# Optimization experiments

Measured on AMD Instinct MI355X. Metric: run time of the kernel, lower is better.

## Reference

```python
import jax, jax.numpy as jnp
import numpy as np

N, T, CIN = 40000, 32, 8
VW = 64          # back_voxelwise_channels
P = 16           # v2b_maxvoxels (voxels stacked per BEV cell)
BEV_H, BEV_W = 496, 432
EPS = 1e-5


def _bn(key, shape):
    # returns stacked (gamma, beta, running_mean, running_var) along axis -2
    k1, k2, k3 = jax.random.split(key, 3)
    g = 1.0 + 0.1 * jax.random.normal(k1, shape, jnp.float32)
    b = 0.1 * jax.random.normal(k2, shape, jnp.float32)
    m = 0.1 * jax.random.normal(k3, shape, jnp.float32)
    v = jnp.ones(shape, jnp.float32)
    return jnp.stack([g, b, m, v], axis=-2)


def setup_inputs() -> dict:
    key = jax.random.key(0)
    ks = jax.random.split(key, 20)
    features = jax.random.normal(ks[0], (N, T, CIN), jnp.float32)
    cy = jax.random.randint(ks[1], (N, 1), 0, BEV_H)
    cx = jax.random.randint(ks[2], (N, 1), 0, BEV_W)
    coors = jnp.concatenate([cy, cx], axis=1).astype(jnp.int32)
    num_voxels = jax.random.randint(ks[3], (N,), 1, T + 1).astype(jnp.int32)

    def w(k, o, i):
        return jax.random.normal(k, (o, i), jnp.float32) / float(np.sqrt(i))

    return dict(
        features=features, coors=coors, num_voxels=num_voxels,
        vfe1_W=w(ks[4], 8, CIN), vfe1_bn=_bn(ks[5], (8,)),
        vfe2_W=w(ks[6], 32, 16), vfe2_bn=_bn(ks[7], (32,)),
        vfe3_W=w(ks[8], 64, 64), vfe3_bn=_bn(ks[9], (64,)),
        vfe4_W=w(ks[10], 64, 64), vfe4_bn=_bn(ks[11], (64,)),
        bfe1_W=jax.random.normal(ks[12], (16, P, P), jnp.float32) / float(np.sqrt(P)),
        bfe1_bn=_bn(ks[13], (16, P)),
        bfe2_W=jax.random.normal(ks[14], (16, 2, P), jnp.float32) / float(np.sqrt(P)),
        bfe2_bn=_bn(ks[15], (16, 2)),
        bfe3_W=w(ks[16], 128, 128), bfe3_bn=_bn(ks[17], (128,)),
    )


def _forward(features, vfe1_W, vfe1_bn, vfe2_W, vfe2_bn, vfe3_W, vfe3_bn,
             vfe4_W, vfe4_bn, bfe1_W, bfe1_bn, bfe2_W, bfe2_bn, bfe3_W, bfe3_bn,
             coors, num_voxels):
    n, t = features.shape[0], features.shape[1]
    f32 = features.dtype
    mask = (jnp.arange(t)[None, :] < num_voxels[:, None]).astype(f32)[..., None]  # [N,T,1]

    def fe(x, W, bn):  # Linear (no bias) + BatchNorm1d (eval) + Mish
        g, b, m, v = bn
        y = x @ W.T
        y = (y - m) * jax.lax.rsqrt(v + EPS) * g + b
        return y * jnp.tanh(jax.nn.softplus(y))

    def vfe(x, W, bn):  # pointwise FE, max-pool over points, concat
        p = fe(x, W, bn)
        agg = jnp.max(p, axis=1, keepdims=True)
        return jnp.concatenate([p, jnp.broadcast_to(agg, p.shape)], axis=2)

    x1 = vfe(features, vfe1_W, vfe1_bn)           # [N,T,16]
    x2 = vfe(x1, vfe2_W, vfe2_bn) * mask          # [N,T,64]
    x3 = fe(x2, vfe3_W, vfe3_bn)
    x4 = fe(x3, vfe4_W, vfe4_bn) * mask + x2
    voxelwise = jnp.max(x4, axis=1)               # [N,64]

    # ---- voxel2bev: group voxels by BEV cell, stack up to P per cell ----
    cell = coors[:, 0] * BEV_W + coors[:, 1]                         # [N]
    ucell, inv = jnp.unique(cell, return_inverse=True, size=n, fill_value=BEV_H * BEV_W)
    order = jnp.argsort(inv)                                          # stable
    inv_sorted = inv[order]
    pos_sorted = jnp.arange(n) - jnp.searchsorted(inv_sorted, inv_sorted, side='left')
    slot = jnp.zeros(n, jnp.int32).at[order].set(pos_sorted.astype(jnp.int32))
    row = jnp.where(slot < P, inv, n)                                 # overflow -> dropped
    bevs = jnp.zeros((n, P, VW), f32).at[row, jnp.minimum(slot, P - 1)].set(
        voxelwise, mode='drop')                                       # [N,P,64]
    counts = jax.ops.segment_sum(jnp.ones(n, jnp.int32), inv, num_segments=n)
    numv = jnp.minimum(counts, P)
    bevcoors = jnp.stack([ucell // BEV_W, ucell % BEV_W], axis=1)     # [N,2]

    # ---- 16 grouped FE stacks over the slot dimension ----
    x0 = bevs.transpose(0, 2, 1).reshape(n, 16, 4, P)                 # [N,16,4,P]
    m2 = (jnp.arange(P)[None, :] < numv[:, None]).astype(f32)[:, None, None, :]
    y = jnp.einsum('ngip,gqp->ngiq', x0, bfe1_W)                      # [N,16,4,P]
    g1, b1, m1, v1 = (bfe1_bn[None, :, i, None, :] for i in range(4))
    y = (y - m1) * jax.lax.rsqrt(v1 + EPS) * g1 + b1
    y = y * jnp.tanh(jax.nn.softplus(y)) * m2
    z = jnp.einsum('ngip,gcp->ngic', y, bfe2_W)                       # [N,16,4,2]
    g2, b2, m2b, v2 = (bfe2_bn[None, :, i, None, :] for i in range(4))
    z = (z - m2b) * jax.lax.rsqrt(v2 + EPS) * g2 + b2
    z = z * jnp.tanh(jax.nn.softplus(z))
    # torch cat along dim=-1 then view -> layout [N, 4, 16, 2] flattened
    x17 = z.transpose(0, 2, 1, 3).reshape(n, 128)
    x18 = fe(x17, bfe3_W, bfe3_bn)
    x19 = fe(x18, bfe3_W, bfe3_bn)   # original applies bfe3 twice (bfe4 unused)

    bevmap = jnp.zeros((BEV_H, BEV_W, 128), f32).at[
        bevcoors[:, 0], bevcoors[:, 1]].set(x19, mode='drop')
    return bevmap.transpose(2, 1, 0)                                  # [128, W, H]


def reference(features, coors, num_voxels, vfe1_W, vfe1_bn, vfe2_W, vfe2_bn,
              vfe3_W, vfe3_bn, vfe4_W, vfe4_bn, bfe1_W, bfe1_bn, bfe2_W, bfe2_bn,
              bfe3_W, bfe3_bn):
    return _forward(features, vfe1_W, vfe1_bn, vfe2_W, vfe2_bn, vfe3_W, vfe3_bn,
                    vfe4_W, vfe4_bn, bfe1_W, bfe1_bn, bfe2_W, bfe2_bn,
                    bfe3_W, bfe3_bn, coors, num_voxels)
```

## Files before the change

### kernel.cpp

```cpp
#include <hip/hip_runtime.h>

#define BEVW 432
#define BEVH 496
#define NCELL (BEVW*BEVH)
#define NVOX  40000
#define EPSB  1e-5f

typedef float f32x2 __attribute__((ext_vector_type(2)));
typedef float f32x4 __attribute__((ext_vector_type(4)));
typedef unsigned int u32x4 __attribute__((ext_vector_type(4)));
typedef short bf16x8 __attribute__((ext_vector_type(8)));

#define REP8_0(M)  M(0) M(1) M(2) M(3) M(4) M(5) M(6) M(7)
#define REP8_8(M)  M(8) M(9) M(10) M(11) M(12) M(13) M(14) M(15)
#define REP16_0(M)  REP8_0(M)  REP8_8(M)


__device__ __forceinline__ float mishf(float y) {
    float e = __expf(fminf(y, 40.f));
    float n = e * (e + 2.f);
    return y * n * __builtin_amdgcn_rcpf(n + 2.f);
}

template <int CTRL>
__device__ __forceinline__ float dppmaxf(float a) {
    int p = __builtin_amdgcn_update_dpp(0, __float_as_int(a), CTRL, 0xF, 0xF, true);
    return fmaxf(a, __int_as_float(p));
}
#define WMAX32(a) { \
    a = dppmaxf<0xB1>(a); \
    a = dppmaxf<0x4E>(a); \
    a = dppmaxf<0x141>(a); \
    a = dppmaxf<0x140>(a); \
    a = fmaxf(a, __int_as_float(__builtin_amdgcn_ds_swizzle(__float_as_int(a), 0x401F))); }

__device__ __forceinline__ bf16x8 mkbf8(uint a, uint b, uint c, uint d) {
    u32x4 t = {a, b, c, d};
    return __builtin_bit_cast(bf16x8, t);
}

__device__ __forceinline__ uint splitbf(float x) {
    uint rh = __float_as_uint(x) & 0xFFFF0000u;
    float lof = x - __uint_as_float(rh);
    uint ul = __float_as_uint(lof);
    uint rl = (ul + 0x7FFFu + ((ul >> 16) & 1u)) >> 16;
    return (rh >> 16) | (rl << 16);
}

__global__ __launch_bounds__(256) void setup_kernel(
    const float* __restrict__ vbn1, const float* __restrict__ vbn2,
    const float* __restrict__ vbn3, const float* __restrict__ vbn4,
    const float* __restrict__ bbn1, const float* __restrict__ bbn2,
    const float* __restrict__ bbn3, const float* __restrict__ W4,
    const float* __restrict__ W3g, const float* __restrict__ W2g,
    float* __restrict__ fold, ushort* __restrict__ w4fh, ushort* __restrict__ w4fl,
    ushort* __restrict__ w3fh, ushort* __restrict__ w3fl,
    ushort* __restrict__ w2fh, ushort* __restrict__ w2fl)
{
    int tid = threadIdx.x;
    if (tid < 8)  { float s = vbn1[tid]/sqrtf(vbn1[24+tid]+EPSB);  fold[tid]      = s; fold[8+tid]   = vbn1[8+tid]  - vbn1[16+tid]*s; }
    if (tid < 32) { float s = vbn2[tid]/sqrtf(vbn2[96+tid]+EPSB);  fold[16+tid]   = s; fold[48+tid]  = vbn2[32+tid] - vbn2[64+tid]*s; }
    if (tid < 64) { float s = vbn3[tid]/sqrtf(vbn3[192+tid]+EPSB); fold[80+tid]   = s; fold[144+tid] = vbn3[64+tid] - vbn3[128+tid]*s; }
    if (tid < 64) { float s = vbn4[tid]/sqrtf(vbn4[192+tid]+EPSB); fold[208+tid]  = s; fold[272+tid] = vbn4[64+tid] - vbn4[128+tid]*s; }
    if (tid < 128){ float s = bbn3[tid]/sqrtf(bbn3[384+tid]+EPSB); fold[336+tid]  = s; fold[464+tid] = bbn3[128+tid]- bbn3[256+tid]*s; }
    { int g = tid >> 4, q = tid & 15;
      const float* b = bbn1 + g*64;
      float s = b[q]/sqrtf(b[48+q]+EPSB);
      fold[592+tid] = s; fold[848+tid] = b[16+q] - b[32+q]*s; }
    if (tid < 32) { int g = tid >> 1, c = tid & 1;
      const float* b = bbn2 + g*8;
      float s = b[c]/sqrtf(b[6+c]+EPSB);
      fold[1104+tid] = s; fold[1136+tid] = b[2+c] - b[4+c]*s; }

    for (int i = tid; i < 4096; i += 256) {
        int j = i & 7, ln = (i >> 3) & 63, nt = (i >> 9) & 3, kc = i >> 11;
        int n = (ln & 15) + nt*16;
        int k = kc*32 + (ln >> 4)*8 + j;
        {
            float val = W4[n*64 + k];
            uint u = splitbf(val);
            w4fh[i] = (ushort)(u & 0xFFFFu);
            w4fl[i] = (ushort)(u >> 16);
        }
        {
            float val = W3g[n*64 + k];
            uint u = splitbf(val);
            w3fh[i] = (ushort)(u & 0xFFFFu);
            w3fl[i] = (ushort)(u >> 16);
        }
    }

    for (int i = tid; i < 1024; i += 256) {
        int j = i & 7, ln = (i >> 3) & 63, nt = (i >> 9) & 1;
        int n = (ln & 15) + nt*16;
        int k = (ln >> 4)*8 + j;
        float val = (k < 16) ? W2g[n*16 + k] : 0.f;
        uint u = splitbf(val);
        w2fh[i] = (ushort)(u & 0xFFFFu);
        w2fl[i] = (ushort)(u >> 16);
    }
}

#define MF3(D, AH, AL, BH, BL) \
    D = __builtin_amdgcn_mfma_f32_16x16x32_bf16(AL, BH, D, 0, 0, 0); \
    D = __builtin_amdgcn_mfma_f32_16x16x32_bf16(AH, BL, D, 0, 0, 0); \
    D = __builtin_amdgcn_mfma_f32_16x16x32_bf16(AH, BH, D, 0, 0, 0);

#define LDA(SRCP, mt, AH, AL) { \
    const uint* ap_ = (SRCP) + ((lane & 15) + 16*(mt))*33 + quad*8; \
    uint u0 = ap_[0], u1 = ap_[1], u2 = ap_[2], u3 = ap_[3]; \
    uint u4 = ap_[4], u5 = ap_[5], u6 = ap_[6], u7 = ap_[7]; \
    AH = mkbf8(__builtin_amdgcn_perm(u1,u0,0x05040100), __builtin_amdgcn_perm(u3,u2,0x05040100), \
               __builtin_amdgcn_perm(u5,u4,0x05040100), __builtin_amdgcn_perm(u7,u6,0x05040100)); \
    AL = mkbf8(__builtin_amdgcn_perm(u1,u0,0x07060302), __builtin_amdgcn_perm(u3,u2,0x07060302), \
               __builtin_amdgcn_perm(u5,u4,0x07060302), __builtin_amdgcn_perm(u7,u6,0x07060302)); }

#define LDA2(SRCP, mt, AH, AL) { \
    const uint* ap_ = (SRCP) + ((lane & 15) + 16*(mt))*33 + (quad & 1)*8; \
    uint u0 = ap_[0], u1 = ap_[1], u2 = ap_[2], u3 = ap_[3]; \
    uint u4 = ap_[4], u5 = ap_[5], u6 = ap_[6], u7 = ap_[7]; \
    AH = mkbf8(__builtin_amdgcn_perm(u1,u0,0x05040100), __builtin_amdgcn_perm(u3,u2,0x05040100), \
               __builtin_amdgcn_perm(u5,u4,0x05040100), __builtin_amdgcn_perm(u7,u6,0x05040100)); \
    AL = mkbf8(__builtin_amdgcn_perm(u1,u0,0x07060302), __builtin_amdgcn_perm(u3,u2,0x07060302), \
               __builtin_amdgcn_perm(u5,u4,0x07060302), __builtin_amdgcn_perm(u7,u6,0x07060302)); }

#define LDB8(ARR, BHP, BLP) { \
    uint4 h0_=(BHP)[0], l0_=(BLP)[0], h1_=(BHP)[64], l1_=(BLP)[64]; \
    uint4 h2_=(BHP)[128], l2_=(BLP)[128], h3_=(BHP)[192], l3_=(BLP)[192]; \
    ARR[0]=mkbf8(h0_.x,h0_.y,h0_.z,h0_.w); ARR[1]=mkbf8(l0_.x,l0_.y,l0_.z,l0_.w); \
    ARR[2]=mkbf8(h1_.x,h1_.y,h1_.z,h1_.w); ARR[3]=mkbf8(l1_.x,l1_.y,l1_.z,l1_.w); \
    ARR[4]=mkbf8(h2_.x,h2_.y,h2_.z,h2_.w); ARR[5]=mkbf8(l2_.x,l2_.y,l2_.z,l2_.w); \
    ARR[6]=mkbf8(h3_.x,h3_.y,h3_.z,h3_.w); ARR[7]=mkbf8(l3_.x,l3_.y,l3_.z,l3_.w); }

#define TILE4A(SRCP, mt, BA, D0, D1, D2, D3) { \
    bf16x8 Ah_, Al_; LDA(SRCP, mt, Ah_, Al_) \
    MF3(D0, Ah_, Al_, BA[0], BA[1]) MF3(D1, Ah_, Al_, BA[2], BA[3]) \
    MF3(D2, Ah_, Al_, BA[4], BA[5]) MF3(D3, Ah_, Al_, BA[6], BA[7]) }

#define DOSETA(SRCP, BA, ACC, SKA, SKB) { \
    TILE4A(SRCP, 0, BA, ACC[0], ACC[1], ACC[2], ACC[3]) \
    TILE4A(SRCP, 2, BA, ACC[8], ACC[9], ACC[10], ACC[11]) \
    if (!(SKA)) { TILE4A(SRCP, 1, BA, ACC[4], ACC[5], ACC[6], ACC[7]) } \
    if (!(SKB)) { TILE4A(SRCP, 3, BA, ACC[12], ACC[13], ACC[14], ACC[15]) } }

__global__ __launch_bounds__(64, 3) void vfe_kernel(
    const float* __restrict__ feat, const int* __restrict__ coors,
    const int* __restrict__ nvx,
    const float* __restrict__ W1,
    const ushort* __restrict__ w2fh, const ushort* __restrict__ w2fl,
    const ushort* __restrict__ w3fh, const ushort* __restrict__ w3fl,
    const ushort* __restrict__ w4fh, const ushort* __restrict__ w4fl,
    const float* __restrict__ fold,
    float* __restrict__ voxelwise, int* __restrict__ cnt,
    int* __restrict__ list, int* __restrict__ nact, int* __restrict__ act)
{
    __shared__ char ldsbuf[16896];
    int tid = threadIdx.x;
    int lane = tid;
    int quad = lane >> 4;
    int c0 = lane & 15;
    int v = blockIdx.x * 2 + (tid >> 5);
    int vA = blockIdx.x * 2;
    int t = tid & 31;
    uint*  x2s  = (uint*)ldsbuf;
    uint*  x2s1 = x2s + 2112;

    const float* fp = feat + (v*32 + t)*8;
    float4 fa = *(const float4*)(fp);
    float4 fb = *(const float4*)(fp+4);
    int numv = nvx[v];
    bf16x8 Bw2[4];
    {
        const uint4* bh2 = (const uint4*)w2fh + lane;
        const uint4* bl2 = (const uint4*)w2fl + lane;
        uint4 h0_=bh2[0], l0_=bl2[0], h1_=bh2[64], l1_=bl2[64];
        Bw2[0]=mkbf8(h0_.x,h0_.y,h0_.z,h0_.w); Bw2[1]=mkbf8(l0_.x,l0_.y,l0_.z,l0_.w);
        Bw2[2]=mkbf8(h1_.x,h1_.y,h1_.z,h1_.w); Bw2[3]=mkbf8(l1_.x,l1_.y,l1_.z,l1_.w);
    }

#define D1(o) float x1_##o; float m1_##o;
    REP8_0(D1)
#undef D1
#define FE1(o) { const float* w = W1 + (o)*8; \
    float ya = fa.x*w[0] + fa.y*w[1]; float yb = fa.z*w[2] + fa.w*w[3]; \
    float yc = fb.x*w[4] + fb.y*w[5]; float yd = fb.z*w[6] + fb.w*w[7]; \
    float yy = ((ya+yb)+(yc+yd)) * fold[(o)] + fold[8+(o)]; \
    x1_##o = mishf(yy); }
    REP8_0(FE1)
#undef FE1
#define P1(o) { float a = x1_##o; WMAX32(a); m1_##o = a; }
    REP8_0(P1)
#undef P1

    int nA = __builtin_amdgcn_readfirstlane(__shfl(numv, 0));
    int nB = __builtin_amdgcn_readfirstlane(__shfl(numv, 32));
    const bool skipA = (nA <= 16);
    const bool skipB = (nB <= 16);

#define S1(o) { x2s1[lane*33 + (o)] = splitbf(x1_##o); x2s1[lane*33 + 8 + (o)] = splitbf(m1_##o); }
    REP8_0(S1)
#undef S1

    bf16x8 BA[8], BB[8];
    {
        const uint4* bh3 = (const uint4*)w3fh + lane;
        const uint4* bl3 = (const uint4*)w3fl + lane;
        LDB8(BA, bh3, bl3)
    }

    f32x4 f2[8];
#pragma unroll
    for (int i = 0; i < 8; i++) f2[i] = (f32x4){0.f,0.f,0.f,0.f};
    {
        { bf16x8 Ah_,Al_; LDA2(x2s1,0,Ah_,Al_) MF3(f2[0],Ah_,Al_,Bw2[0],Bw2[1]) MF3(f2[1],Ah_,Al_,Bw2[2],Bw2[3]) }
        { bf16x8 Ah_,Al_; LDA2(x2s1,1,Ah_,Al_) MF3(f2[2],Ah_,Al_,Bw2[0],Bw2[1]) MF3(f2[3],Ah_,Al_,Bw2[2],Bw2[3]) }
        { bf16x8 Ah_,Al_; LDA2(x2s1,2,Ah_,Al_) MF3(f2[4],Ah_,Al_,Bw2[0],Bw2[1]) MF3(f2[5],Ah_,Al_,Bw2[2],Bw2[3]) }
        { bf16x8 Ah_,Al_; LDA2(x2s1,3,Ah_,Al_) MF3(f2[6],Ah_,Al_,Bw2[0],Bw2[1]) MF3(f2[7],Ah_,Al_,Bw2[2],Bw2[3]) }
    }

    {
        const uint4* bh3 = (const uint4*)w3fh + 256 + lane;
        const uint4* bl3 = (const uint4*)w3fl + 256 + lane;
        LDB8(BB, bh3, bl3)
    }

    float s2a = fold[16+c0], t2a = fold[48+c0];
    float s2b = fold[32+c0], t2b = fold[64+c0];
#define MSH4(s, SS, TT) { f2[s].x=mishf(f2[s].x*(SS)+(TT)); f2[s].y=mishf(f2[s].y*(SS)+(TT)); \
                          f2[s].z=mishf(f2[s].z*(SS)+(TT)); f2[s].w=mishf(f2[s].w*(SS)+(TT)); }
    MSH4(0,s2a,t2a) MSH4(1,s2b,t2b) MSH4(2,s2a,t2a) MSH4(3,s2b,t2b)
    MSH4(4,s2a,t2a) MSH4(5,s2b,t2b) MSH4(6,s2a,t2a) MSH4(7,s2b,t2b)
#undef MSH4

#define MX4(V) fmaxf(fmaxf((V).x,(V).y), fmaxf((V).z,(V).w))
    float aggA0 = fmaxf(MX4(f2[0]), MX4(f2[2]));
    float aggA1 = fmaxf(MX4(f2[1]), MX4(f2[3]));
    float aggB0 = fmaxf(MX4(f2[4]), MX4(f2[6]));
    float aggB1 = fmaxf(MX4(f2[5]), MX4(f2[7]));
#undef MX4
#define REDQ(p) p = fmaxf(p, __shfl_xor(p, 16)); p = fmaxf(p, __shfl_xor(p, 32));
    REDQ(aggA0) REDQ(aggA1) REDQ(aggB0) REDQ(aggB1)
#undef REDQ
    uint sgA0 = splitbf(aggA0), sgA1 = splitbf(aggA1);
    uint sgB0 = splitbf(aggB0), sgB1 = splitbf(aggB1);

#define ST2(mt, NVV, SG0, SG1) { \
    int rt_ = quad*4 + 16*((mt)&1); \
    int gr_ = (quad*4 + 16*(mt))*33; \
    float m0_=(rt_+0<(NVV))?1.f:0.f, m1_=(rt_+1<(NVV))?1.f:0.f; \
    float m2_=(rt_+2<(NVV))?1.f:0.f, m3_=(rt_+3<(NVV))?1.f:0.f; \
    f32x4 a_ = f2[(mt)*2], b_ = f2[(mt)*2+1]; \
    x2s[gr_    + c0] = splitbf(a_.x*m0_);  x2s[gr_    + c0+16] = splitbf(b_.x*m0_); \
    x2s[gr_+33 + c0] = splitbf(a_.y*m1_);  x2s[gr_+33 + c0+16] = splitbf(b_.y*m1_); \
    x2s[gr_+66 + c0] = splitbf(a_.z*m2_);  x2s[gr_+66 + c0+16] = splitbf(b_.z*m2_); \
    x2s[gr_+99 + c0] = splitbf(a_.w*m3_);  x2s[gr_+99 + c0+16] = splitbf(b_.w*m3_); \
    x2s1[gr_    + c0] = (m0_!=0.f)?(SG0):0u;  x2s1[gr_    + c0+16] = (m0_!=0.f)?(SG1):0u; \
    x2s1[gr_+33 + c0] = (m1_!=0.f)?(SG0):0u;  x2s1[gr_+33 + c0+16] = (m1_!=0.f)?(SG1):0u; \
    x2s1[gr_+66 + c0] = (m2_!=0.f)?(SG0):0u;  x2s1[gr_+66 + c0+16] = (m2_!=0.f)?(SG1):0u; \
    x2s1[gr_+99 + c0] = (m3_!=0.f)?(SG0):0u;  x2s1[gr_+99 + c0+16] = (m3_!=0.f)?(SG1):0u; }
    ST2(0, nA, sgA0, sgA1)
    ST2(2, nB, sgB0, sgB1)
    if (!skipA) { ST2(1, nA, sgA0, sgA1) }
    if (!skipB) { ST2(3, nB, sgB0, sgB1) }
#undef ST2

    f32x4 e[16];
#define EIN(i) e[i] = (f32x4){0.f,0.f,0.f,0.f};
    REP16_0(EIN)
#undef EIN
    DOSETA(x2s,  BA, e, skipA, skipB)
    DOSETA(x2s1, BB, e, skipA, skipB)

    {
        const uint4* bh4 = (const uint4*)w4fh + lane;
        const uint4* bl4 = (const uint4*)w4fl + lane;
        LDB8(BA, bh4, bl4)
    }

    uint* x3st = x2s1;
    f32x4 d[16];
#define DIN(i) d[i] = (f32x4){0.f,0.f,0.f,0.f};
    REP16_0(DIN)
#undef DIN

#define POST(TI, mt, nt) { \
    float s_ = fold[80 + c0 + 16*(nt)], tb_ = fold[144 + c0 + 16*(nt)]; \
    int col_ = c0 + 16*((nt)&1); \
    int rowb_ = quad*4 + 16*(mt); \
    x3st[(rowb_+0)*33 + col_] = splitbf(mishf(e[TI].x * s_ + tb_)); \
    x3st[(rowb_+1)*33 + col_] = splitbf(mishf(e[TI].y * s_ + tb_)); \
    x3st[(rowb_+2)*33 + col_] = splitbf(mishf(e[TI].z * s_ + tb_)); \
    x3st[(rowb_+3)*33 + col_] = splitbf(mishf(e[TI].w * s_ + tb_)); }

    {
        POST(0,0,0)  POST(1,0,1)
        POST(8,2,0)  POST(9,2,1)
        if (!skipA) { POST(4,1,0)  POST(5,1,1) }
        if (!skipB) { POST(12,3,0) POST(13,3,1) }
        DOSETA(x3st, BA, d, skipA, skipB)
    }
    {
        const uint4* bh4 = (const uint4*)w4fh + 256 + lane;
        const uint4* bl4 = (const uint4*)w4fl + 256 + lane;
        LDB8(BB, bh4, bl4)
    }
    {
        POST(2,0,2)  POST(3,0,3)
        POST(10,2,2) POST(11,2,3)
        if (!skipA) { POST(6,1,2)  POST(7,1,3) }
        if (!skipB) { POST(14,3,2) POST(15,3,3) }
        DOSETA(x3st, BB, d, skipA, skipB)
    }
#undef POST

    float s0f = fold[208+c0],    t0f = fold[272+c0];
    float s1f = fold[208+16+c0], t1f = fold[272+16+c0];
    float s2f = fold[208+32+c0], t2f = fold[272+32+c0];
    float s3f = fold[208+48+c0], t3f = fold[272+48+c0];
    float piA = skipA ? 0.f : -3.4e38f;
    float piB = skipB ? 0.f : -3.4e38f;
    float pA0=piA, pA1=piA, pA2=piA, pA3=piA;
    float pB0=piB, pB1=piB, pB2=piB, pB3=piB;

#define RECON(u) (__uint_as_float((u)<<16) + __uint_as_float((u) & 0xFFFF0000u))
#define FTP(D, mt, nt, SS, TT, PV) { \
    int nv = ((mt) >> 1) ? nB : nA; \
    int rf = quad*4 + 16*(mt); \
    int rt = quad*4 + 16*((mt)&1); \
    int cb = c0 + 16*(nt); \
    float m0=(rt+0<nv)?1.f:0.f, m1=(rt+1<nv)?1.f:0.f, m2=(rt+2<nv)?1.f:0.f, m3=(rt+3<nv)?1.f:0.f; \
    uint ua_ = x2s[(rf+0)*33 + cb], ub_ = x2s[(rf+1)*33 + cb]; \
    uint uc_ = x2s[(rf+2)*33 + cb], ud_ = x2s[(rf+3)*33 + cb]; \
    float y0 = mishf(D.x*SS + TT)*m0 + RECON(ua_); \
    float y1 = mishf(D.y*SS + TT)*m1 + RECON(ub_); \
    float y2 = mishf(D.z*SS + TT)*m2 + RECON(uc_); \
    float y3 = mishf(D.w*SS + TT)*m3 + RECON(ud_); \
    PV = fmaxf(PV, fmaxf(fmaxf(y0,y1), fmaxf(y2,y3))); }

#define FTA(D, mt, nt, SS, TT, AG, PV) { \
    int nv = ((mt) >> 1) ? nB : nA; \
    int rt = quad*4 + 16*((mt)&1); \
    float m0=(rt+0<nv)?1.f:0.f, m1=(rt+1<nv)?1.f:0.f, m2=(rt+2<nv)?1.f:0.f, m3=(rt+3<nv)?1.f:0.f; \
    float y0 = (mishf(D.x*SS + TT) + AG)*m0; \
    float y1 = (mishf(D.y*SS + TT) + AG)*m1; \
    float y2 = (mishf(D.z*SS + TT) + AG)*m2; \
    float y3 = (mishf(D.w*SS + TT) + AG)*m3; \
    PV = fmaxf(PV, fmaxf(fmaxf(y0,y1), fmaxf(y2,y3))); }

    FTP(d[0], 0, 0, s0f, t0f, pA0)  FTP(d[1], 0, 1, s1f, t1f, pA1)
    FTA(d[2], 0, 2, s2f, t2f, aggA0, pA2)  FTA(d[3], 0, 3, s3f, t3f, aggA1, pA3)
    if (!skipA) {
        FTP(d[4], 1, 0, s0f, t0f, pA0)  FTP(d[5], 1, 1, s1f, t1f, pA1)
        FTA(d[6], 1, 2, s2f, t2f, aggA0, pA2)  FTA(d[7], 1, 3, s3f, t3f, aggA1, pA3)
    }
    FTP(d[8], 2, 0, s0f, t0f, pB0)  FTP(d[9], 2, 1, s1f, t1f, pB1)
    FTA(d[10], 2, 2, s2f, t2f, aggB0, pB2)  FTA(d[11], 2, 3, s3f, t3f, aggB1, pB3)
    if (!skipB) {
        FTP(d[12], 3, 0, s0f, t0f, pB0)  FTP(d[13], 3, 1, s1f, t1f, pB1)
        FTA(d[14], 3, 2, s2f, t2f, aggB0, pB2)  FTA(d[15], 3, 3, s3f, t3f, aggB1, pB3)
    }
#undef FTP
#undef FTA
#undef RECON

#define RED(p) p = fmaxf(p, __shfl_xor(p, 16)); p = fmaxf(p, __shfl_xor(p, 32));
    RED(pA0) RED(pA1) RED(pA2) RED(pA3) RED(pB0) RED(pB1) RED(pB2) RED(pB3)
#undef RED

    if (quad == 0) {
        float* vwA = voxelwise + vA*64;
        vwA[c0] = pA0; vwA[c0+16] = pA1; vwA[c0+32] = pA2; vwA[c0+48] = pA3;
        float* vwB = voxelwise + (vA+1)*64;
        vwB[c0] = pB0; vwB[c0+16] = pB1; vwB[c0+32] = pB2; vwB[c0+48] = pB3;
    }

    if (t == 0) {
        int cell = coors[v*2] * BEVW + coors[v*2+1];
        int pos = atomicAdd(&cnt[cell], 1);
        if (pos < 16) list[cell*16 + pos] = v;
        if (pos == 0) { int k = atomicAdd(nact, 1); act[k] = cell; }
    }
}

__global__ __launch_bounds__(256) void bfe_front(
    const int* __restrict__ nact, const int* __restrict__ act,
    const int* __restrict__ cnt, const int* __restrict__ list,
    const float* __restrict__ voxelwise,
    const float* __restrict__ W1g, const float* __restrict__ W2g,
    const float* __restrict__ fold, float* __restrict__ x17g,
    int* __restrict__ idx)
{
    int n_act = *nact;
    int aidx = blockIdx.x * 4 + (threadIdx.x >> 6);
    if (aidx >= n_act) return;

    int lane = threadIdx.x & 63;
    int g = lane >> 2, ii = lane & 3;
    int cell = act[aidx];
    int numv = min(cnt[cell], 16);
    if (lane == 0) idx[cell] = aidx + 1;

    int myidx = (lane < numv) ? list[cell*16 + lane] : (0x40000000 + lane);
    int rank = 0;
    for (int j = 0; j < numv; j++) { int vj = __shfl(myidx, j); rank += (vj < myidx) ? 1 : 0; }
    if (lane >= numv) rank = lane;
    int sorted = __builtin_amdgcn_ds_permute(rank << 2, myidx);

#define YD(q) float y_##q = 0.f;
    REP16_0(YD)
#undef YD
    for (int p = 0; p < numv; p++) {
        int sv = __shfl(sorted, p);
        float val = voxelwise[sv*64 + lane];
        const float* w = W1g + g*256 + p;
#define BF1(q) y_##q += val * w[(q)*16];
        REP16_0(BF1)
#undef BF1
    }
#define BN1(q) { float yy = y_##q * fold[592 + g*16 + (q)] + fold[848 + g*16 + (q)]; \
    yy = mishf(yy); y_##q = ((q) < numv) ? yy : 0.f; }
    REP16_0(BN1)
#undef BN1

    float z0 = 0.f, z1 = 0.f;
#define BF2(p) z0 += y_##p * W2g[g*32 + (p)]; z1 += y_##p * W2g[g*32 + 16 + (p)];
    REP16_0(BF2)
#undef BF2
    z0 = mishf(z0 * fold[1104 + g*2 + 0] + fold[1136 + g*2 + 0]);
    z1 = mishf(z1 * fold[1104 + g*2 + 1] + fold[1136 + g*2 + 1]);

    int k0 = ii*32 + g*2;
    *(float2*)(x17g + aidx*128 + k0) = make_float2(z0, z1);
}

__global__ __launch_bounds__(512, 4) void bfe3_fused(
    const int* __restrict__ nactp,
    const float* __restrict__ W3, const float* __restrict__ fold,
    float* __restrict__ x17g)
{
    __shared__ float XL[64*128];
    int tid = threadIdx.x;
    int n_act = *nactp;
    int cb = blockIdx.x * 64;

    for (int i = tid; i < 64*32; i += 512) {
        int c = i >> 5, kc = i & 31;
        float4 val = (cb + c < n_act) ? ((const float4*)x17g)[(size_t)(cb+c)*32 + kc]
                                      : make_float4(0.f,0.f,0.f,0.f);
        ((float4*)XL)[c*32 + (kc ^ (c & 31))] = val;
    }
    __syncthreads();

    int wv = __builtin_amdgcn_readfirstlane(tid >> 6);
    int c  = tid & 63;
    int ob = wv * 16;
    int cswz = c & 31;
    const float4* xrow = (const float4*)XL + c*32;
    const float4* W4p = (const float4*)W3;

#define DECLB(q) f32x2 ap_##q = {0.f, 0.f};
#define ACCB(q) { const f32x2* wp_ = (const f32x2*)(W4p + (ob+(q))*32 + kc); \
    ap_##q += xv01 * wp_[0]; ap_##q += xv23 * wp_[1]; }
#define ACTB(q) float a_##q; { float yy = (ap_##q.x + ap_##q.y) * fold[336+ob+(q)] + fold[464+ob+(q)]; a_##q = mishf(yy); }
    {
        REP16_0(DECLB)
        for (int kc = 0; kc < 32; kc++) {
            float4 xv = xrow[kc ^ cswz];
            f32x2 xv01 = {xv.x, xv.y}, xv23 = {xv.z, xv.w};
            REP16_0(ACCB)
        }
        REP16_0(ACTB)
        __syncthreads();
        ((float4*)XL)[c*32 + ((wv*4 + 0) ^ cswz)] = make_float4(a_0,  a_1,  a_2,  a_3);
        ((float4*)XL)[c*32 + ((wv*4 + 1) ^ cswz)] = make_float4(a_4,  a_5,  a_6,  a_7);
        ((float4*)XL)[c*32 + ((wv*4 + 2) ^ cswz)] = make_float4(a_8,  a_9,  a_10, a_11);
        ((float4*)XL)[c*32 + ((wv*4 + 3) ^ cswz)] = make_float4(a_12, a_13, a_14, a_15);
    }
    __syncthreads();

    {
        const float4* yrow = (const float4*)XL + c*32;
        REP16_0(DECLB)
        for (int kc = 0; kc < 32; kc++) {
            float4 xv = yrow[kc ^ cswz];
            f32x2 xv01 = {xv.x, xv.y}, xv23 = {xv.z, xv.w};
            REP16_0(ACCB)
        }
        REP16_0(ACTB)
        float4* dst = (float4*)(x17g + (size_t)(cb + c)*128 + ob);
        dst[0] = make_float4(a_0,  a_1,  a_2,  a_3);
        dst[1] = make_float4(a_4,  a_5,  a_6,  a_7);
        dst[2] = make_float4(a_8,  a_9,  a_10, a_11);
        dst[3] = make_float4(a_12, a_13, a_14, a_15);
    }
#undef DECLB
#undef ACCB
#undef ACTB
}

__global__ __launch_bounds__(512, 2) void bev_write(
    const int* __restrict__ idx, const float* __restrict__ x19c,
    float* __restrict__ out)
{
    __shared__ float XT[128*65];
    int bid = blockIdx.x;
    int cx = bid % BEVW;
    int cy0 = (bid / BEVW) << 6;
    int tid = threadIdx.x;

    int cell_l = tid >> 3;
    int chq = (tid & 7) << 4;
    int cy = cy0 + cell_l;
    float4 v0 = make_float4(0.f,0.f,0.f,0.f), v1 = v0, v2 = v0, v3 = v0;
    if (cy < BEVH) {
        int ai = idx[cy*BEVW + cx] - 1;
        if (ai >= 0) {
            const float4* src = (const float4*)(x19c + (size_t)ai*128 + chq);
            v0 = src[0]; v1 = src[1]; v2 = src[2]; v3 = src[3];
        }
    }
    float* d = XT + chq*65 + cell_l;
    d[0*65]=v0.x;  d[1*65]=v0.y;  d[2*65]=v0.z;  d[3*65]=v0.w;
    d[4*65]=v1.x;  d[5*65]=v1.y;  d[6*65]=v1.z;  d[7*65]=v1.w;
    d[8*65]=v2.x;  d[9*65]=v2.y;  d[10*65]=v2.z; d[11*65]=v2.w;
    d[12*65]=v3.x; d[13*65]=v3.y; d[14*65]=v3.z; d[15*65]=v3.w;
    __syncthreads();

    int wv2 = tid >> 6, lane = tid & 63;
    int cyw = cy0 + lane;
    if (cyw < BEVH) {
        float* op = out + cx*BEVH + cyw;
#pragma unroll
        for (int k = 0; k < 16; k++) {
            int c = (wv2 << 4) + k;
            op[(size_t)c*NCELL] = XT[c*65 + lane];
        }
    }
}

extern "C" void kernel_launch(void* const* d_in, const int* in_sizes, int n_in,
                              void* d_out, int out_size, void* d_ws, size_t ws_size,
                              hipStream_t stream) {
    const float* features = (const float*)d_in[0];
    const int*   coors    = (const int*)d_in[1];
    const int*   num_vox  = (const int*)d_in[2];
    const float* vfe1_W   = (const float*)d_in[3];
    const float* vfe1_bn  = (const float*)d_in[4];
    const float* vfe2_W   = (const float*)d_in[5];
    const float* vfe2_bn  = (const float*)d_in[6];
    const float* vfe3_W   = (const float*)d_in[7];
    const float* vfe3_bn  = (const float*)d_in[8];
    const float* vfe4_W   = (const float*)d_in[9];
    const float* vfe4_bn  = (const float*)d_in[10];
    const float* bfe1_W   = (const float*)d_in[11];
    const float* bfe1_bn  = (const float*)d_in[12];
    const float* bfe2_W   = (const float*)d_in[13];
    const float* bfe2_bn  = (const float*)d_in[14];
    const float* bfe3_W   = (const float*)d_in[15];
    const float* bfe3_bn  = (const float*)d_in[16];
    float* out = (float*)d_out;

    char* ws = (char*)d_ws;
    int*    nact      = (int*)ws;
    int*    cnt       = (int*)(ws + 256);
    int*    idx       = (int*)(ws + 857344);
    int*    list      = (int*)(ws + 1714432);
    float*  voxelwise = (float*)(ws + 15427840);
    int*    act       = (int*)(ws + 25667840);
    float*  x17g      = (float*)(ws + 25827840);
    float*  fold      = (float*)(ws + 46307840);
    ushort* w4fh      = (ushort*)(ws + 46312512);
    ushort* w4fl      = (ushort*)(ws + 46320704);
    ushort* w3fh      = (ushort*)(ws + 46328896);
    ushort* w3fl      = (ushort*)(ws + 46337088);
    ushort* w2fh      = (ushort*)(ws + 46345280);
    ushort* w2fl      = (ushort*)(ws + 46347328);

    (void)hipMemsetAsync(ws, 0, 1714432, stream);

    setup_kernel<<<1, 256, 0, stream>>>(vfe1_bn, vfe2_bn, vfe3_bn, vfe4_bn,
                                        bfe1_bn, bfe2_bn, bfe3_bn, vfe4_W, vfe3_W, vfe2_W,
                                        fold, w4fh, w4fl, w3fh, w3fl, w2fh, w2fl);
    vfe_kernel<<<NVOX/2, 64, 0, stream>>>(features, coors, num_vox,
                                          vfe1_W, w2fh, w2fl, w3fh, w3fl, w4fh, w4fl, fold,
                                          voxelwise, cnt, list, nact, act);
    bfe_front<<<NVOX/4, 256, 0, stream>>>(nact, act, cnt, list, voxelwise,
                                          bfe1_W, bfe2_W, fold, x17g, idx);
    bfe3_fused<<<(NVOX+63)/64, 512, 0, stream>>>(nact, bfe3_W, fold, x17g);
    bev_write<<<BEVW*8, 512, 0, stream>>>(idx, x17g, out);
}
```

Measured before the change: 507.5 us.

## Fuse BEV front stage with bfe3 layers and use split-bf16 MFMA

Merges the per-cell bfe1/bfe2 front kernel into the bfe3 kernel, so the 128-wide x17 features stay in shared memory instead of going through global memory. The two 128x128 bfe3 matmuls switch from fp32 FMA loops to MFMA using a split-bf16 (hi/lo) representation that keeps near-fp32 accuracy. This removes a kernel launch and a global round trip of x17. In exchange, each wave now processes 8 cells serially in the front stage, which reduces parallelism there, and the output stores become strided scalar writes.

```diff
diff --git a/kernel.cpp b/kernel.cpp
--- a/kernel.cpp
+++ b/kernel.cpp
@@ -382,120 +382,128 @@
     }
 }
 
-__global__ __launch_bounds__(256) void bfe_front(
-    const int* __restrict__ nact, const int* __restrict__ act,
+__global__ __launch_bounds__(512) void bfe_back(
+    const int* __restrict__ nactp, const int* __restrict__ act,
     const int* __restrict__ cnt, const int* __restrict__ list,
     const float* __restrict__ voxelwise,
     const float* __restrict__ W1g, const float* __restrict__ W2g,
-    const float* __restrict__ fold, float* __restrict__ x17g,
-    int* __restrict__ idx)
+    const float* __restrict__ W3, const float* __restrict__ fold,
+    float* __restrict__ x17g, int* __restrict__ idx)
 {
-    int n_act = *nact;
-    int aidx = blockIdx.x * 4 + (threadIdx.x >> 6);
-    if (aidx >= n_act) return;
-
-    int lane = threadIdx.x & 63;
-    int g = lane >> 2, ii = lane & 3;
-    int cell = act[aidx];
-    int numv = min(cnt[cell], 16);
-    if (lane == 0) idx[cell] = aidx + 1;
-
-    int myidx = (lane < numv) ? list[cell*16 + lane] : (0x40000000 + lane);
-    int rank = 0;
-    for (int j = 0; j < numv; j++) { int vj = __shfl(myidx, j); rank += (vj < myidx) ? 1 : 0; }
-    if (lane >= numv) rank = lane;
-    int sorted = __builtin_amdgcn_ds_permute(rank << 2, myidx);
-
-#define YD(q) float y_##q = 0.f;
-    REP16_0(YD)
-#undef YD
-    for (int p = 0; p < numv; p++) {
-        int sv = __shfl(sorted, p);
-        float val = voxelwise[sv*64 + lane];
-        const float* w = W1g + g*256 + p;
-#define BF1(q) y_##q += val * w[(q)*16];
-        REP16_0(BF1)
-#undef BF1
-    }
-#define BN1(q) { float yy = y_##q * fold[592 + g*16 + (q)] + fold[848 + g*16 + (q)]; \
-    yy = mishf(yy); y_##q = ((q) < numv) ? yy : 0.f; }
-    REP16_0(BN1)
-#undef BN1
-
-    float z0 = 0.f, z1 = 0.f;
-#define BF2(p) z0 += y_##p * W2g[g*32 + (p)]; z1 += y_##p * W2g[g*32 + 16 + (p)];
-    REP16_0(BF2)
-#undef BF2
-    z0 = mishf(z0 * fold[1104 + g*2 + 0] + fold[1136 + g*2 + 0]);
-    z1 = mishf(z1 * fold[1104 + g*2 + 1] + fold[1136 + g*2 + 1]);
-
-    int k0 = ii*32 + g*2;
-    *(float2*)(x17g + aidx*128 + k0) = make_float2(z0, z1);
-}
-
-__global__ __launch_bounds__(512, 4) void bfe3_fused(
-    const int* __restrict__ nactp,
-    const float* __restrict__ W3, const float* __restrict__ fold,
-    float* __restrict__ x17g)
-{
-    __shared__ float XL[64*128];
+    __shared__ uint XA[4*2112];
     int tid = threadIdx.x;
     int n_act = *nactp;
     int cb = blockIdx.x * 64;
-
-    for (int i = tid; i < 64*32; i += 512) {
-        int c = i >> 5, kc = i & 31;
-        float4 val = (cb + c < n_act) ? ((const float4*)x17g)[(size_t)(cb+c)*32 + kc]
-                                      : make_float4(0.f,0.f,0.f,0.f);
-        ((float4*)XL)[c*32 + (kc ^ (c & 31))] = val;
+    int wv = tid >> 6;
+    int lane = tid & 63;
+    int quad = lane >> 4, c0 = lane & 15;
+    int g = lane >> 2, ii = lane & 3;
+
+    for (int r = 0; r < 8; r++) {
+        int ci = (wv << 3) + r;
+        int aidx = cb + ci;
+        uint z0u = 0u, z1u = 0u;
+        if (aidx < n_act) {
+            int cell = act[aidx];
+            int numv = min(cnt[cell], 16);
+            if (lane == 0) idx[cell] = aidx + 1;
+            int myidx = (lane < numv) ? list[cell*16 + lane] : (0x40000000 + lane);
+            int rank = 0;
+            for (int j = 0; j < numv; j++) { int vj = __shfl(myidx, j); rank += (vj < myidx) ? 1 : 0; }
+            if (lane >= numv) rank = lane;
+            int sorted = __builtin_amdgcn_ds_permute(rank << 2, myidx);
+
+#define YD(q) float y_##q = 0.f;
+            REP16_0(YD)
+#undef YD
+            for (int p = 0; p < numv; p++) {
+                int sv = __shfl(sorted, p);
+                float val = voxelwise[sv*64 + lane];
+                const float* w = W1g + g*256 + p;
+#define BF1(q) y_##q += val * w[(q)*16];
+                REP16_0(BF1)
+#undef BF1
+            }
+#define BN1(q) { float yy = y_##q * fold[592 + g*16 + (q)] + fold[848 + g*16 + (q)]; \
+    yy = mishf(yy); y_##q = ((q) < numv) ? yy : 0.f; }
+            REP16_0(BN1)
+#undef BN1
+            float z0 = 0.f, z1 = 0.f;
+#define BF2(p) z0 += y_##p * W2g[g*32 + (p)]; z1 += y_##p * W2g[g*32 + 16 + (p)];
+            REP16_0(BF2)
+#undef BF2
+            z0 = mishf(z0 * fold[1104 + g*2 + 0] + fold[1136 + g*2 + 0]);
+            z1 = mishf(z1 * fold[1104 + g*2 + 1] + fold[1136 + g*2 + 1]);
+            z0u = splitbf(z0); z1u = splitbf(z1);
+        }
+        XA[ii*2112 + ci*33 + g*2]     = z0u;
+        XA[ii*2112 + ci*33 + g*2 + 1] = z1u;
     }
     __syncthreads();
 
-    int wv = __builtin_amdgcn_readfirstlane(tid >> 6);
-    int c  = tid & 63;
-    int ob = wv * 16;
-    int cswz = c & 31;
-    const float4* xrow = (const float4*)XL + c*32;
-    const float4* W4p = (const float4*)W3;
-
-#define DECLB(q) f32x2 ap_##q = {0.f, 0.f};
-#define ACCB(q) { const f32x2* wp_ = (const f32x2*)(W4p + (ob+(q))*32 + kc); \
-    ap_##q += xv01 * wp_[0]; ap_##q += xv23 * wp_[1]; }
-#define ACTB(q) float a_##q; { float yy = (ap_##q.x + ap_##q.y) * fold[336+ob+(q)] + fold[464+ob+(q)]; a_##q = mishf(yy); }
-    {
-        REP16_0(DECLB)
-        for (int kc = 0; kc < 32; kc++) {
-            float4 xv = xrow[kc ^ cswz];
-            f32x2 xv01 = {xv.x, xv.y}, xv23 = {xv.z, xv.w};
-            REP16_0(ACCB)
-        }
-        REP16_0(ACTB)
-        __syncthreads();
-        ((float4*)XL)[c*32 + ((wv*4 + 0) ^ cswz)] = make_float4(a_0,  a_1,  a_2,  a_3);
-        ((float4*)XL)[c*32 + ((wv*4 + 1) ^ cswz)] = make_float4(a_4,  a_5,  a_6,  a_7);
-        ((float4*)XL)[c*32 + ((wv*4 + 2) ^ cswz)] = make_float4(a_8,  a_9,  a_10, a_11);
-        ((float4*)XL)[c*32 + ((wv*4 + 3) ^ cswz)] = make_float4(a_12, a_13, a_14, a_15);
-    }
+    int nch = c0 + (wv << 4);
+    float s5 = fold[336 + nch], t5 = fold[464 + nch];
+#define BLD(KC) bf16x8 B3h##KC, B3l##KC; { \
+    const float* wr = W3 + nch*128 + (KC)*32 + quad*8; \
+    float4 wa = *(const float4*)wr; float4 wb = *(const float4*)(wr+4); \
+    uint u0=splitbf(wa.x), u1=splitbf(wa.y), u2=splitbf(wa.z), u3=splitbf(wa.w); \
+    uint u4=splitbf(wb.x), u5=splitbf(wb.y), u6=splitbf(wb.z), u7=splitbf(wb.w); \
+    B3h##KC = mkbf8(__builtin_amdgcn_perm(u1,u0,0x05040100), __builtin_amdgcn_perm(u3,u2,0x05040100), \
+                    __builtin_amdgcn_perm(u5,u4,0x05040100), __builtin_amdgcn_perm(u7,u6,0x05040100)); \
+    B3l##KC = mkbf8(__builtin_amdgcn_perm(u1,u0,0x07060302), __builtin_amdgcn_perm(u3,u2,0x07060302), \
+                    __builtin_amdgcn_perm(u5,u4,0x07060302), __builtin_amdgcn_perm(u7,u6,0x07060302)); }
+    BLD(0) BLD(1) BLD(2) BLD(3)
+#undef BLD
+
+#define KSTEP(KC, Q0, Q1, Q2, Q3) { \
+    const uint* ch_ = XA + (KC)*2112; \
+    bf16x8 Ah0,Al0,Ah1,Al1,Ah2,Al2,Ah3,Al3; \
+    LDA(ch_,0,Ah0,Al0) LDA(ch_,1,Ah1,Al1) LDA(ch_,2,Ah2,Al2) LDA(ch_,3,Ah3,Al3) \
+    MF3(Q0,Ah0,Al0,B3h##KC,B3l##KC) MF3(Q1,Ah1,Al1,B3h##KC,B3l##KC) \
+    MF3(Q2,Ah2,Al2,B3h##KC,B3l##KC) MF3(Q3,Ah3,Al3,B3h##KC,B3l##KC) }
+
+#define PASS3(Q0,Q1,Q2,Q3) \
+    Q0 = (f32x4){0.f,0.f,0.f,0.f}; Q1 = Q0; Q2 = Q0; Q3 = Q0; \
+    KSTEP(0,Q0,Q1,Q2,Q3) KSTEP(1,Q0,Q1,Q2,Q3) KSTEP(2,Q0,Q1,Q2,Q3) KSTEP(3,Q0,Q1,Q2,Q3)
+
+#define ACT4(Q) { Q.x = mishf(Q.x*s5+t5); Q.y = mishf(Q.y*s5+t5); \
+                  Q.z = mishf(Q.z*s5+t5); Q.w = mishf(Q.w*s5+t5); }
+
+    f32x4 q0, q1, q2, q3;
+    PASS3(q0,q1,q2,q3)
+    ACT4(q0) ACT4(q1) ACT4(q2) ACT4(q3)
     __syncthreads();
-
-    {
-        const float4* yrow = (const float4*)XL + c*32;
-        REP16_0(DECLB)
-        for (int kc = 0; kc < 32; kc++) {
-            float4 xv = yrow[kc ^ cswz];
-            f32x2 xv01 = {xv.x, xv.y}, xv23 = {xv.z, xv.w};
-            REP16_0(ACCB)
-        }
-        REP16_0(ACTB)
-        float4* dst = (float4*)(x17g + (size_t)(cb + c)*128 + ob);
-        dst[0] = make_float4(a_0,  a_1,  a_2,  a_3);
-        dst[1] = make_float4(a_4,  a_5,  a_6,  a_7);
-        dst[2] = make_float4(a_8,  a_9,  a_10, a_11);
-        dst[3] = make_float4(a_12, a_13, a_14, a_15);
-    }
-#undef DECLB
-#undef ACCB
-#undef ACTB
+    {
+        uint* dst = XA + (wv >> 1)*2112 + ((wv & 1) << 4) + c0;
+        int rb = quad*4;
+        dst[(rb+0)*33]      = splitbf(q0.x); dst[(rb+1)*33]      = splitbf(q0.y);
+        dst[(rb+2)*33]      = splitbf(q0.z); dst[(rb+3)*33]      = splitbf(q0.w);
+        dst[(rb+16)*33]     = splitbf(q1.x); dst[(rb+17)*33]     = splitbf(q1.y);
+        dst[(rb+18)*33]     = splitbf(q1.z); dst[(rb+19)*33]     = splitbf(q1.w);
+        dst[(rb+32)*33]     = splitbf(q2.x); dst[(rb+33)*33]     = splitbf(q2.y);
+        dst[(rb+34)*33]     = splitbf(q2.z); dst[(rb+35)*33]     = splitbf(q2.w);
+        dst[(rb+48)*33]     = splitbf(q3.x); dst[(rb+49)*33]     = splitbf(q3.y);
+        dst[(rb+50)*33]     = splitbf(q3.z); dst[(rb+51)*33]     = splitbf(q3.w);
+    }
+    __syncthreads();
+
+    PASS3(q0,q1,q2,q3)
+    ACT4(q0) ACT4(q1) ACT4(q2) ACT4(q3)
+#undef ACT4
+#undef PASS3
+#undef KSTEP
+
+    {
+        size_t rb = (size_t)(cb + quad*4);
+        x17g[(rb+0)*128 + nch] = q0.x;  x17g[(rb+1)*128 + nch] = q0.y;
+        x17g[(rb+2)*128 + nch] = q0.z;  x17g[(rb+3)*128 + nch] = q0.w;
+        x17g[(rb+16)*128 + nch] = q1.x; x17g[(rb+17)*128 + nch] = q1.y;
+        x17g[(rb+18)*128 + nch] = q1.z; x17g[(rb+19)*128 + nch] = q1.w;
+        x17g[(rb+32)*128 + nch] = q2.x; x17g[(rb+33)*128 + nch] = q2.y;
+        x17g[(rb+34)*128 + nch] = q2.z; x17g[(rb+35)*128 + nch] = q2.w;
+        x17g[(rb+48)*128 + nch] = q3.x; x17g[(rb+49)*128 + nch] = q3.y;
+        x17g[(rb+50)*128 + nch] = q3.z; x17g[(rb+51)*128 + nch] = q3.w;
+    }
 }
 
 __global__ __launch_bounds__(512, 2) void bev_write(
@@ -584,8 +592,7 @@
     vfe_kernel<<<NVOX/2, 64, 0, stream>>>(features, coors, num_vox,
                                           vfe1_W, w2fh, w2fl, w3fh, w3fl, w4fh, w4fl, fold,
                                           voxelwise, cnt, list, nact, act);
-    bfe_front<<<NVOX/4, 256, 0, stream>>>(nact, act, cnt, list, voxelwise,
-                                          bfe1_W, bfe2_W, fold, x17g, idx);
-    bfe3_fused<<<(NVOX+63)/64, 512, 0, stream>>>(nact, bfe3_W, fold, x17g);
+    bfe_back<<<(NVOX+63)/64, 512, 0, stream>>>(nact, act, cnt, list, voxelwise,
+                                               bfe1_W, bfe2_W, bfe3_W, fold, x17g, idx);
     bev_write<<<BEVW*8, 512, 0, stream>>>(idx, x17g, out);
 }
```

Result: no change. 511.0 us (+0.7%).
